# Kernel tuning notes

Measured on AMD Instinct MI355X. Metric: run time of the kernel, lower is better.

The kernel has to match this reference:

```python
import jax, jax.numpy as jnp
import numpy as np

N_NODES = 50000
N_EDGES = 800000
DIM = 256


def setup_inputs() -> dict:
    key = jax.random.key(0)
    k1, k2, k3, k4 = jax.random.split(key, 4)
    x = jax.random.normal(k1, (N_NODES, DIM), dtype=jnp.float32)
    edge_index = jax.random.randint(k2, (2, N_EDGES), 0, N_NODES, dtype=jnp.int64)
    # GCNConv learned params (glorot-style weight, zero bias like PyG default init)
    W = jax.random.normal(k3, (DIM, DIM), dtype=jnp.float32) * (1.0 / np.sqrt(DIM))
    b = jnp.zeros((DIM,), dtype=jnp.float32)
    return {"x": x, "edge_index": edge_index, "W": W, "b": b}


def reference(x, edge_index, W, b):
    # GNNBlock forward (eval mode: dropout is identity; normalizer=Identity,
    # activation=ReLU, projection=Identity since in_dim==out_dim).
    n = x.shape[0]
    # --- GCNConv with self-loops and symmetric normalization ---
    loop = jnp.arange(n, dtype=edge_index.dtype)
    src = jnp.concatenate([edge_index[0], loop])  # [E+N]
    dst = jnp.concatenate([edge_index[1], loop])  # [E+N]
    ones = jnp.ones(src.shape[0], dtype=x.dtype)
    deg = jax.ops.segment_sum(ones, dst, num_segments=n)  # in-degree incl. self-loop
    dinv = jnp.where(deg > 0, jax.lax.rsqrt(deg), 0.0)
    norm = dinv[src] * dinv[dst]  # [E+N]
    h = x @ W  # transform first (in->out), then aggregate
    msg = h[src] * norm[:, None]  # gather + scale, [E+N, DIM]
    agg = jax.ops.segment_sum(msg, dst, num_segments=n) + b  # scatter-add
    # --- norm (Identity) -> activation (ReLU) -> residual -> dropout (eval) ---
    out = jax.nn.relu(agg) + x
    return out
```

## Files before the change

kernel.cpp:

```cpp
#include <hip/hip_runtime.h>

#define N_NODES 50000
#define DIM 256
#define NBUCK 196
#define BCAP 6144
#define CEDGES 2048
#define MSTRIDE 512
#define APAD 264
#define EPAD 260
#define TROWS 16

typedef __attribute__((ext_vector_type(8))) short bf16x8;
typedef __attribute__((ext_vector_type(4))) float f32x4;
typedef __attribute__((ext_vector_type(2))) float f32x2;
union U16 { uint4 u; bf16x8 s; };

__device__ __forceinline__ unsigned short f2b(float f) {
    unsigned int u = __float_as_uint(f);
    return (unsigned short)((u + 0x7FFFu + ((u >> 16) & 1u)) >> 16);
}

__global__ __launch_bounds__(256) void coarse_kernel(const int* __restrict__ src,
                                                     const int* __restrict__ dst, int E,
                                                     unsigned int* __restrict__ slab2,
                                                     int* __restrict__ meta_t) {
    __shared__ int hist[NBUCK];
    __shared__ int scn[NBUCK];
    __shared__ int cur[NBUCK];
    __shared__ int s2[256];
    __shared__ unsigned int sorted[CEDGES];

    const int tid = threadIdx.x;
    const int e0 = blockIdx.x * CEDGES;
    const int nE = min(CEDGES, E - e0);

    if (tid < NBUCK) hist[tid] = 0;
    __syncthreads();

    unsigned int pk[8];
    #pragma unroll
    for (int i = 0; i < 8; ++i) {
        int idx = i * 256 + tid;
        pk[i] = 0xFFFFFFFFu;
        if (idx < nE) {
            unsigned int s = (unsigned int)src[e0 + idx];
            unsigned int d = (unsigned int)dst[e0 + idx];
            pk[i] = (d << 16) | s;
            atomicAdd(&hist[d >> 8], 1);
        }
    }
    __syncthreads();

    int v = (tid < NBUCK) ? hist[tid] : 0;
    s2[tid] = v;
    __syncthreads();
    for (int off = 1; off < 256; off <<= 1) {
        int t = (tid >= off) ? s2[tid - off] : 0;
        __syncthreads();
        s2[tid] += t;
        __syncthreads();
    }
    if (tid < NBUCK) {
        scn[tid] = s2[tid] - v;
        cur[tid] = 0;
    }
    __syncthreads();

    #pragma unroll
    for (int i = 0; i < 8; ++i) {
        if (pk[i] != 0xFFFFFFFFu) {
            int bkt = pk[i] >> 24;
            int p = scn[bkt] + atomicAdd(&cur[bkt], 1);
            sorted[p] = pk[i];
        }
    }
    __syncthreads();

    for (int i = tid; i < nE; i += 256)
        slab2[(size_t)blockIdx.x * CEDGES + i] = sorted[i];
    if (tid < NBUCK)
        meta_t[tid * MSTRIDE + blockIdx.x] = (scn[tid] << 16) | (hist[tid] & 0xFFFF);
}

__global__ __launch_bounds__(1024) void fine_prep_kernel(int nCoarse,
                                                         const unsigned int* __restrict__ slab2,
                                                         const int* __restrict__ meta_t,
                                                         int* __restrict__ offs,
                                                         int* __restrict__ deg,
                                                         float* __restrict__ dinv,
                                                         int* __restrict__ csr_src,
                                                         const float* __restrict__ W,
                                                         uint4* __restrict__ Bpack,
                                                         const float* __restrict__ x,
                                                         unsigned int* __restrict__ xq) {
    __shared__ int rcnt[512];
    __shared__ int rst[512];
    __shared__ int rbase[512];
    __shared__ int scn[256];
    __shared__ int hist[256];
    __shared__ unsigned short rmap[BCAP];
    __shared__ unsigned int stage[BCAP];

    const int tid = threadIdx.x;

    if (blockIdx.x >= NBUCK) {
        int role = blockIdx.x - NBUCK;
        if (role < 8) {
            int gid  = role * 1024 + tid;
            int lane = gid & 63;
            int u    = (gid >> 6) & 15;
            int ki   = gid >> 10;
            int n    = u * 16 + (lane & 15);
            int k0   = ki * 32 + (lane >> 4) * 8;
            unsigned int w[4];
            #pragma unroll
            for (int p = 0; p < 4; ++p) {
                unsigned int lo = f2b(W[(size_t)(k0 + 2 * p) * DIM + n]);
                unsigned int hi = f2b(W[(size_t)(k0 + 2 * p + 1) * DIM + n]);
                w[p] = lo | (hi << 16);
            }
            Bpack[gid] = make_uint4(w[0], w[1], w[2], w[3]);
        } else {
            int gid = (role - 8) * 1024 + tid;
            float4 v = ((const float4*)x)[gid];
            int p = __builtin_amdgcn_cvt_pk_fp8_f32(v.x, v.y, 0, false);
            p     = __builtin_amdgcn_cvt_pk_fp8_f32(v.z, v.w, p, true);
            xq[gid] = (unsigned int)p;
        }
        return;
    }

    const int g = blockIdx.x;

    if (tid < 512) {
        if (tid < nCoarse) {
            int m = meta_t[g * MSTRIDE + tid];
            rcnt[tid] = m & 0xFFFF;
            rst[tid]  = (m >> 16) & 0xFFFF;
        } else {
            rcnt[tid] = 0;
        }
    }
    if (tid < 256) hist[tid] = 0;
    __syncthreads();

    int c0 = 0, ps = 0;
    if (tid < 256) {
        c0 = rcnt[2 * tid];
        ps = c0 + rcnt[2 * tid + 1];
        scn[tid] = ps;
    }
    __syncthreads();
    for (int off = 1; off < 256; off <<= 1) {
        int t = (tid < 256 && tid >= off) ? scn[tid - off] : 0;
        __syncthreads();
        if (tid < 256) scn[tid] += t;
        __syncthreads();
    }
    if (tid < 256) {
        int pexcl = scn[tid] - ps;
        rbase[2 * tid]     = pexcl;
        rbase[2 * tid + 1] = pexcl + c0;
    }
    __syncthreads();
    const int total = scn[255];
    const int cnt = min(total, BCAP);

    if (tid < 512) {
        int n = rcnt[tid], b0 = rbase[tid];
        for (int k = 0; k < n; ++k)
            if (b0 + k < BCAP) rmap[b0 + k] = (unsigned short)tid;
    }
    __syncthreads();

    for (int e = tid; e < cnt; e += 1024) {
        int r = rmap[e];
        unsigned int p = slab2[(size_t)r * CEDGES + rst[r] + (e - rbase[r])];
        stage[e] = p;
        atomicAdd(&hist[(p >> 16) & 255], 1);
    }
    __syncthreads();

    int d = 0;
    if (tid < 256) {
        d = hist[tid];
        scn[tid] = d;
    }
    __syncthreads();
    for (int off = 1; off < 256; off <<= 1) {
        int t = (tid < 256 && tid >= off) ? scn[tid - off] : 0;
        __syncthreads();
        if (tid < 256) scn[tid] += t;
        __syncthreads();
    }
    const int base = g * BCAP;
    if (tid < 256) {
        int excl = scn[tid] - d;
        int node = g * 256 + tid;
        if (node < N_NODES) {
            offs[node] = base + excl;
            deg[node]  = d;
            dinv[node] = rsqrtf((float)(d + 1));
        }
        hist[tid] = excl;
    }
    __syncthreads();

    for (int e = tid; e < cnt; e += 1024) {
        unsigned int p = stage[e];
        int pos = atomicAdd(&hist[(p >> 16) & 255], 1);
        csr_src[base + pos] = (int)(p & 0xFFFFu);
    }
}

__global__ __launch_bounds__(256) void agg_gemm_kernel(const unsigned int* __restrict__ xq,
                                                       const int* __restrict__ offs,
                                                       const int* __restrict__ deg,
                                                       const int* __restrict__ csr_src,
                                                       const float* __restrict__ dinv,
                                                       const float* __restrict__ x,
                                                       const uint4* __restrict__ Bpack,
                                                       const float* __restrict__ b,
                                                       float* __restrict__ out) {
    __shared__ __align__(16) char LDSraw[TROWS * EPAD * 4];
    ushort* ALDS = (ushort*)LDSraw;
    float*  ELDS = (float*)LDSraw;

    const int tid  = threadIdx.x;
    const int wave = tid >> 6;
    const int lane = tid & 63;
    const int row0 = blockIdx.x * TROWS;

    for (int j = 0; j < 4; ++j) {
        const int r   = wave * 4 + j;
        const int row = row0 + r;
        ushort4 st4 = make_ushort4(0, 0, 0, 0);
        if (row < N_NODES) {
            const float di = dinv[row];
            unsigned int qself = xq[(size_t)row * 64 + lane];
            f32x2 lo = __builtin_amdgcn_cvt_pk_f32_fp8((int)qself, false);
            f32x2 hi = __builtin_amdgcn_cvt_pk_f32_fp8((int)qself, true);
            float ax = lo.x * di, ay = lo.y * di, az = hi.x * di, aw = hi.y * di;

            const int start = offs[row];
            const int n     = deg[row];
            int i = 0;
            for (; i + 8 <= n; i += 8) {
                int s0 = csr_src[start + i + 0], s1 = csr_src[start + i + 1];
                int s2 = csr_src[start + i + 2], s3 = csr_src[start + i + 3];
                int s4 = csr_src[start + i + 4], s5 = csr_src[start + i + 5];
                int s6 = csr_src[start + i + 6], s7 = csr_src[start + i + 7];
                unsigned int q0 = xq[(size_t)s0 * 64 + lane];
                unsigned int q1 = xq[(size_t)s1 * 64 + lane];
                unsigned int q2 = xq[(size_t)s2 * 64 + lane];
                unsigned int q3 = xq[(size_t)s3 * 64 + lane];
                unsigned int q4 = xq[(size_t)s4 * 64 + lane];
                unsigned int q5 = xq[(size_t)s5 * 64 + lane];
                unsigned int q6 = xq[(size_t)s6 * 64 + lane];
                unsigned int q7 = xq[(size_t)s7 * 64 + lane];
                float d0 = dinv[s0], d1 = dinv[s1], d2 = dinv[s2], d3 = dinv[s3];
                float d4 = dinv[s4], d5 = dinv[s5], d6 = dinv[s6], d7 = dinv[s7];
                #pragma unroll
                for (int u = 0; u < 8; ++u) {
                    unsigned int q; float dd;
                    switch (u) {
                        case 0: q = q0; dd = d0; break; case 1: q = q1; dd = d1; break;
                        case 2: q = q2; dd = d2; break; case 3: q = q3; dd = d3; break;
                        case 4: q = q4; dd = d4; break; case 5: q = q5; dd = d5; break;
                        case 6: q = q6; dd = d6; break; default: q = q7; dd = d7; break;
                    }
                    f32x2 l = __builtin_amdgcn_cvt_pk_f32_fp8((int)q, false);
                    f32x2 h = __builtin_amdgcn_cvt_pk_f32_fp8((int)q, true);
                    ax += l.x * dd; ay += l.y * dd; az += h.x * dd; aw += h.y * dd;
                }
            }
            for (; i < n; ++i) {
                int s = csr_src[start + i];
                unsigned int q = xq[(size_t)s * 64 + lane];
                float dd = dinv[s];
                f32x2 l = __builtin_amdgcn_cvt_pk_f32_fp8((int)q, false);
                f32x2 h = __builtin_amdgcn_cvt_pk_f32_fp8((int)q, true);
                ax += l.x * dd; ay += l.y * dd; az += h.x * dd; aw += h.y * dd;
            }
            ax *= di; ay *= di; az *= di; aw *= di;
            st4 = make_ushort4(f2b(ax), f2b(ay), f2b(az), f2b(aw));
        }
        *(ushort4*)&ALDS[r * APAD + lane * 4] = st4;
    }
    __syncthreads();

    const int m  = lane & 15;
    const int kb = lane >> 4;

    f32x4 acc[4];
    #pragma unroll
    for (int t = 0; t < 4; ++t) acc[t] = (f32x4){0.f, 0.f, 0.f, 0.f};

    const uint4* bp = Bpack + (size_t)(wave * 4) * 64 + lane;

    for (int ki = 0; ki < 8; ++ki) {
        U16 bf[4], af;
        #pragma unroll
        for (int t = 0; t < 4; ++t) bf[t].u = bp[(size_t)(ki * 16 + t) * 64];
        af.u = *(const uint4*)&ALDS[m * APAD + ki * 32 + kb * 8];
        #pragma unroll
        for (int t = 0; t < 4; ++t)
            acc[t] = __builtin_amdgcn_mfma_f32_16x16x32_bf16(af.s, bf[t].s, acc[t], 0, 0, 0);
    }

    __syncthreads();
    #pragma unroll
    for (int t = 0; t < 4; ++t) {
        #pragma unroll
        for (int reg = 0; reg < 4; ++reg) {
            ELDS[(kb * 4 + reg) * EPAD + wave * 64 + t * 16 + m] = acc[t][reg];
        }
    }
    __syncthreads();

    const float4* x4g = (const float4*)x;
    const float4* b4  = (const float4*)b;
    float4* out4 = (float4*)out;

    #pragma unroll
    for (int j = 0; j < 4; ++j) {
        int idx  = j * 256 + tid;
        int lrow = idx >> 6;
        int c4   = idx & 63;
        int grow = row0 + lrow;
        if (grow < N_NODES) {
            float4 v  = *(const float4*)&ELDS[lrow * EPAD + c4 * 4];
            float4 bb = b4[c4];
            float4 xx = x4g[(size_t)grow * 64 + c4];
            float4 o;
            o.x = fmaxf(v.x + bb.x, 0.f) + xx.x;
            o.y = fmaxf(v.y + bb.y, 0.f) + xx.y;
            o.z = fmaxf(v.z + bb.z, 0.f) + xx.z;
            o.w = fmaxf(v.w + bb.w, 0.f) + xx.w;
            out4[(size_t)grow * 64 + c4] = o;
        }
    }
}

extern "C" void kernel_launch(void* const* d_in, const int* in_sizes, int n_in,
                              void* d_out, int out_size, void* d_ws, size_t ws_size,
                              hipStream_t stream) {
    const float* x  = (const float*)d_in[0];
    const int*   ei = (const int*)d_in[1];
    const float* W  = (const float*)d_in[2];
    const float* b  = (const float*)d_in[3];
    float* out = (float*)d_out;
    const int E = in_sizes[1] / 2;

    char* ws = (char*)d_ws;
    int*          deg     = (int*)(ws);
    int*          offs    = (int*)(ws + 262144);
    float*        dinv    = (float*)(ws + 524288);
    int*          csr_src = (int*)(ws + 786432);
    int*          meta_t  = (int*)(ws + 5767168);
    unsigned int* slab2   = (unsigned int*)(ws + 6291456);
    uint4*        Bpack   = (uint4*)(ws + 9699328);
    unsigned int* xq      = (unsigned int*)(ws + 10485760);

    const int* src = ei;
    const int* dst = ei + E;

    const int nCoarse = (E + CEDGES - 1) / CEDGES;
    const int nXq1k = (N_NODES * 64) / 1024;

    coarse_kernel<<<nCoarse, 256, 0, stream>>>(src, dst, E, slab2, meta_t);
    fine_prep_kernel<<<NBUCK + 8 + nXq1k, 1024, 0, stream>>>(nCoarse, slab2, meta_t,
                                                             offs, deg, dinv, csr_src,
                                                             W, Bpack, x, xq);
    agg_gemm_kernel<<<(N_NODES + TROWS - 1) / TROWS, 256, 0, stream>>>(xq, offs, deg, csr_src,
                                                                       dinv, x, Bpack, b, out);
}
```

Measured before the change: 184.5 us.

## Use 16 waves per block, one row and one output tile each

The fused aggregate+GEMM kernel now launches 1024 threads per block instead of 256. Each wave aggregates exactly one node row rather than four, computes one 16-column MFMA tile instead of four, and writes one float4 per thread in the epilogue. This exposes more independent gather latency per block and spreads the irregular per-row neighbour loops across more waves. In exchange, blocks are larger and each wave loads its own B fragments with less reuse, and larger blocks may limit occupancy flexibility.

Result: slower. 205.5 us (+11.4%).

```diff
diff --git a/kernel.cpp b/kernel.cpp
--- a/kernel.cpp
+++ b/kernel.cpp
@@ -213,15 +213,15 @@
     }
 }
 
-__global__ __launch_bounds__(256) void agg_gemm_kernel(const unsigned int* __restrict__ xq,
-                                                       const int* __restrict__ offs,
-                                                       const int* __restrict__ deg,
-                                                       const int* __restrict__ csr_src,
-                                                       const float* __restrict__ dinv,
-                                                       const float* __restrict__ x,
-                                                       const uint4* __restrict__ Bpack,
-                                                       const float* __restrict__ b,
-                                                       float* __restrict__ out) {
+__global__ __launch_bounds__(1024) void agg_gemm_kernel(const unsigned int* __restrict__ xq,
+                                                        const int* __restrict__ offs,
+                                                        const int* __restrict__ deg,
+                                                        const int* __restrict__ csr_src,
+                                                        const float* __restrict__ dinv,
+                                                        const float* __restrict__ x,
+                                                        const uint4* __restrict__ Bpack,
+                                                        const float* __restrict__ b,
+                                                        float* __restrict__ out) {
     __shared__ __align__(16) char LDSraw[TROWS * EPAD * 4];
     ushort* ALDS = (ushort*)LDSraw;
     float*  ELDS = (float*)LDSraw;
@@ -231,9 +231,8 @@
     const int lane = tid & 63;
     const int row0 = blockIdx.x * TROWS;
 
-    for (int j = 0; j < 4; ++j) {
-        const int r   = wave * 4 + j;
-        const int row = row0 + r;
+    {
+        const int row = row0 + wave;
         ushort4 st4 = make_ushort4(0, 0, 0, 0);
         if (row < N_NODES) {
             const float di = dinv[row];
@@ -285,36 +284,25 @@
             ax *= di; ay *= di; az *= di; aw *= di;
             st4 = make_ushort4(f2b(ax), f2b(ay), f2b(az), f2b(aw));
         }
-        *(ushort4*)&ALDS[r * APAD + lane * 4] = st4;
+        *(ushort4*)&ALDS[wave * APAD + lane * 4] = st4;
     }
     __syncthreads();
 
     const int m  = lane & 15;
     const int kb = lane >> 4;
 
-    f32x4 acc[4];
+    f32x4 acc = (f32x4){0.f, 0.f, 0.f, 0.f};
+    for (int ki = 0; ki < 8; ++ki) {
+        U16 bf, af;
+        bf.u = Bpack[(size_t)(ki * 16 + wave) * 64 + lane];
+        af.u = *(const uint4*)&ALDS[m * APAD + ki * 32 + kb * 8];
+        acc = __builtin_amdgcn_mfma_f32_16x16x32_bf16(af.s, bf.s, acc, 0, 0, 0);
+    }
+
+    __syncthreads();
     #pragma unroll
-    for (int t = 0; t < 4; ++t) acc[t] = (f32x4){0.f, 0.f, 0.f, 0.f};
-
-    const uint4* bp = Bpack + (size_t)(wave * 4) * 64 + lane;
-
-    for (int ki = 0; ki < 8; ++ki) {
-        U16 bf[4], af;
-        #pragma unroll
-        for (int t = 0; t < 4; ++t) bf[t].u = bp[(size_t)(ki * 16 + t) * 64];
-        af.u = *(const uint4*)&ALDS[m * APAD + ki * 32 + kb * 8];
-        #pragma unroll
-        for (int t = 0; t < 4; ++t)
-            acc[t] = __builtin_amdgcn_mfma_f32_16x16x32_bf16(af.s, bf[t].s, acc[t], 0, 0, 0);
-    }
-
-    __syncthreads();
-    #pragma unroll
-    for (int t = 0; t < 4; ++t) {
-        #pragma unroll
-        for (int reg = 0; reg < 4; ++reg) {
-            ELDS[(kb * 4 + reg) * EPAD + wave * 64 + t * 16 + m] = acc[t][reg];
-        }
+    for (int reg = 0; reg < 4; ++reg) {
+        ELDS[(kb * 4 + reg) * EPAD + wave * 16 + m] = acc[reg];
     }
     __syncthreads();
 
@@ -322,11 +310,9 @@
     const float4* b4  = (const float4*)b;
     float4* out4 = (float4*)out;
 
-    #pragma unroll
-    for (int j = 0; j < 4; ++j) {
-        int idx  = j * 256 + tid;
-        int lrow = idx >> 6;
-        int c4   = idx & 63;
+    {
+        int lrow = tid >> 6;
+        int c4   = tid & 63;
         int grow = row0 + lrow;
         if (grow < N_NODES) {
             float4 v  = *(const float4*)&ELDS[lrow * EPAD + c4 * 4];
@@ -372,6 +358,6 @@
     fine_prep_kernel<<<NBUCK + 8 + nXq1k, 1024, 0, stream>>>(nCoarse, slab2, meta_t,
                                                              offs, deg, dinv, csr_src,
                                                              W, Bpack, x, xq);
-    agg_gemm_kernel<<<(N_NODES + TROWS - 1) / TROWS, 256, 0, stream>>>(xq, offs, deg, csr_src,
-                                                                       dinv, x, Bpack, b, out);
-}
+    agg_gemm_kernel<<<(N_NODES + TROWS - 1) / TROWS, 1024, 0, stream>>>(xq, offs, deg, csr_src,
+                                                                        dinv, x, Bpack, b, out);
+}
```
